# Kernel optimization log

Hardware: AMD Instinct MI355X
Metric: run time of the kernel (lower is better)

## Reference

```python
import jax, jax.numpy as jnp
import numpy as np

N, D, H, E = 8192, 1024, 4096, 8


def setup_inputs() -> dict:
    key = jax.random.key(0)
    ks = jax.random.split(key, 5)
    s_in = 1.0 / np.sqrt(D)
    s_h = 1.0 / np.sqrt(H)
    return {
        "x": jax.random.normal(ks[0], (N, D), dtype=jnp.float32),
        "Wg": jax.random.normal(ks[1], (D, E), dtype=jnp.float32) * s_in,
        "bg": jnp.zeros((E,), dtype=jnp.float32),
        "W1": jax.random.normal(ks[2], (E, D, H), dtype=jnp.float32) * s_in,
        "b1": jnp.zeros((E, H), dtype=jnp.float32),
        "W2": jax.random.normal(ks[3], (E, H, D), dtype=jnp.float32) * s_h,
        "b2": jnp.zeros((E, D), dtype=jnp.float32),
    }


def reference(x, Wg, bg, W1, b1, W2, b2):
    # gate: softmax linear router -> weights [N, E]
    weights = jax.nn.softmax(x @ Wg + bg, axis=-1)
    # all experts, batched GEMMs: h [N, E, H]
    h = jax.nn.relu(jnp.einsum("nd,edh->neh", x, W1) + b1)  # Dropout is identity at inference
    outputs = jnp.einsum("neh,ehd->ned", h, W2) + b2         # [N, E, D]
    # weighted combine over experts
    return jnp.einsum("ne,ned->nd", weights, outputs)
```

## Files before the change

### kernel.cpp

```cpp
#include <hip/hip_runtime.h>
#include <hip/hip_bf16.h>

#define DDIM 1024
#define HDIM 4096
#define NEXP 8
#define NROW 8192

typedef __attribute__((ext_vector_type(8))) short s16x8;
typedef __attribute__((ext_vector_type(4))) float f32x4;

using bf16 = __hip_bfloat16;

__device__ __forceinline__ void gload16(const bf16* g, bf16* lds) {
    __builtin_amdgcn_global_load_lds(
        (const __attribute__((address_space(1))) unsigned int*)g,
        (__attribute__((address_space(3))) unsigned int*)lds,
        16, 0, 0);
}

template <int N>
__device__ __forceinline__ void wait_vmcnt() {
    if constexpr (N == 6)      asm volatile("s_waitcnt vmcnt(6)" ::: "memory");
    else if constexpr (N == 3) asm volatile("s_waitcnt vmcnt(3)" ::: "memory");
    else                       asm volatile("s_waitcnt vmcnt(0)" ::: "memory");
}

__global__ void cvt_x_kernel(const float* __restrict__ x, bf16* __restrict__ xb, int total4) {
    int i = blockIdx.x * 256 + threadIdx.x;
    if (i >= total4) return;
    float4 v = ((const float4*)x)[i];
    union { bf16 b[4]; uint2 u; } p;
    p.b[0] = __float2bfloat16(v.x);
    p.b[1] = __float2bfloat16(v.y);
    p.b[2] = __float2bfloat16(v.z);
    p.b[3] = __float2bfloat16(v.w);
    ((uint2*)xb)[i] = p.u;
}

__global__ void transpose_cvt_kernel(const float* __restrict__ in, bf16* __restrict__ out,
                                     int R, int C) {
    __shared__ float tile[32][33];
    const size_t esz = (size_t)R * C;
    const float* src = in + (size_t)blockIdx.z * esz;
    bf16* dst = out + (size_t)blockIdx.z * esz;
    int c0 = blockIdx.x * 32, r0 = blockIdx.y * 32;
    int tx = threadIdx.x & 31, ty = threadIdx.x >> 5;
#pragma unroll
    for (int i = 0; i < 32; i += 8)
        tile[ty + i][tx] = src[(size_t)(r0 + ty + i) * C + (c0 + tx)];
    __syncthreads();
#pragma unroll
    for (int i = 0; i < 32; i += 8)
        dst[(size_t)(c0 + ty + i) * R + (r0 + tx)] = __float2bfloat16(tile[tx][ty + i]);
}

__global__ void gate_kernel(const float* __restrict__ x, const float* __restrict__ Wg,
                            const float* __restrict__ bg, float* __restrict__ wts) {
    int wave = threadIdx.x >> 6, lane = threadIdx.x & 63;
    int n = blockIdx.x * 4 + wave;
    const float* xr = x + (size_t)n * DDIM;
    float acc[NEXP] = {0.f, 0.f, 0.f, 0.f, 0.f, 0.f, 0.f, 0.f};
    for (int d = lane; d < DDIM; d += 64) {
        float xv = xr[d];
        const float* wr = Wg + (size_t)d * NEXP;
#pragma unroll
        for (int e = 0; e < NEXP; ++e) acc[e] += xv * wr[e];
    }
#pragma unroll
    for (int off = 32; off > 0; off >>= 1) {
#pragma unroll
        for (int e = 0; e < NEXP; ++e) acc[e] += __shfl_xor(acc[e], off, 64);
    }
    if (lane == 0) {
        float mx = -1e30f;
#pragma unroll
        for (int e = 0; e < NEXP; ++e) { acc[e] += bg[e]; mx = fmaxf(mx, acc[e]); }
        float s = 0.f;
#pragma unroll
        for (int e = 0; e < NEXP; ++e) { acc[e] = __expf(acc[e] - mx); s += acc[e]; }
        float inv = 1.0f / s;
#pragma unroll
        for (int e = 0; e < NEXP; ++e) wts[(size_t)n * NEXP + e] = acc[e] * inv;
    }
}

__global__ void out_init_kernel(const float* __restrict__ wts, const float* __restrict__ b2,
                                float* __restrict__ out) {
    size_t idx = (size_t)blockIdx.x * 256 + threadIdx.x;
    int d = (int)(idx & (DDIM - 1));
    size_t n = idx >> 10;
    const float* w = wts + n * NEXP;
    float s = 0.f;
#pragma unroll
    for (int e = 0; e < NEXP; ++e) s += w[e] * b2[(size_t)e * DDIM + d];
    out[idx] = s;
}

template <int BN, int MODE>
__global__ __launch_bounds__(512, 1) void gemm256(
    const bf16* __restrict__ A, const bf16* __restrict__ BT, void* __restrict__ Cout,
    const float* __restrict__ bias, const float* __restrict__ wts,
    int lda, int ldb, int ldc, int NT, int tilesM, int tilesN, int XGN, int expert) {
    constexpr int WN = BN / 64, WM = 8 / WN;
    constexpr int WROWS = 256 / WM;
    constexpr int MH = WROWS / 64;
    constexpr int HALFA = 256 * 32;
    constexpr int HALFB = BN * 32;
    constexpr int ATOT = 2 * HALFA;
    constexpr int BUFE = ATOT + 2 * HALFB;
    constexpr int BR = BN / 128;
    constexpr int VMC = (BN == 256) ? 6 : 3;
    __shared__ __align__(16) bf16 smem[2 * BUFE];

    const int tid = threadIdx.x;
    const int wave = tid >> 6, lane = tid & 63;
    const int wm = wave / WN, wn = wave % WN;
    const int r = lane & 15, kg = lane >> 4;

    const int xcd = blockIdx.x & 7, slot = blockIdx.x >> 3;
    const int XGM = 8 / XGN;
    const int rm = tilesM / XGM, rn = tilesN / XGN;
    const int g = slot >> 5, u = slot & 31;
    const int gpr = rn >> 3;
    const int gm = (g / gpr) * 4 + (u >> 3);
    const int gn = (g % gpr) * 8 + (u & 7);
    const int tm = (xcd / XGN) * rm + gm;
    const int tn = (xcd % XGN) * rn + gn;

    const bf16* gA = A + (size_t)tm * 256 * lda;
    const bf16* gB = BT + (size_t)tn * BN * ldb;

    f32x4 acc[4 * MH][4];
#pragma unroll
    for (int m = 0; m < 4 * MH; ++m)
#pragma unroll
        for (int n = 0; n < 4; ++n) acc[m][n] = (f32x4){0.f, 0.f, 0.f, 0.f};

    auto stageA = [&](int t, int ks) {
        bf16* dst = smem + (t & 1) * BUFE + ks * HALFA;
#pragma unroll
        for (int j = 0; j < 2; ++j) {
            int c = j * 512 + tid;
            int R = c >> 2, kc = (c & 3) ^ ((R >> 1) & 3);
            gload16(gA + (size_t)R * lda + t * 64 + ks * 32 + kc * 8,
                    dst + (j * 512 + wave * 64) * 8);
        }
    };
    auto stageB = [&](int t, int ks) {
        bf16* dst = smem + (t & 1) * BUFE + ATOT + ks * HALFB;
#pragma unroll
        for (int j = 0; j < BR; ++j) {
            int c = j * 512 + tid;
            int R = c >> 2, kc = (c & 3) ^ ((R >> 1) & 3);
            gload16(gB + (size_t)R * ldb + t * 64 + ks * 32 + kc * 8,
                    dst + (j * 512 + wave * 64) * 8);
        }
    };

    s16x8 a0[4], bb[4];
    auto ldA = [&](int buf, int ks, int mh) {
#pragma unroll
        for (int m = 0; m < 4; ++m) {
            int R = wm * WROWS + mh * 64 + m * 16 + r;
            a0[m] = *(const s16x8*)&smem[buf * BUFE + ks * HALFA + R * 32 +
                                         ((kg ^ ((R >> 1) & 3)) * 8)];
        }
    };
    auto ldB = [&](int buf, int ks) {
#pragma unroll
        for (int n = 0; n < 4; ++n) {
            int R = wn * 64 + n * 16 + r;
            bb[n] = *(const s16x8*)&smem[buf * BUFE + ATOT + ks * HALFB + R * 32 +
                                         ((kg ^ ((R >> 1) & 3)) * 8)];
        }
    };

    auto preMFMA = [&]() {
        __builtin_amdgcn_s_barrier();
        asm volatile("s_waitcnt lgkmcnt(0)" ::: "memory");
        __builtin_amdgcn_sched_barrier(0);
        __builtin_amdgcn_s_setprio(1);
    };
    auto postMFMA = [&](bool vm) {
        __builtin_amdgcn_s_setprio(0);
        if (vm) wait_vmcnt<VMC>();
        __builtin_amdgcn_s_barrier();
    };
    auto mfmaLo = [&]() {
#pragma unroll
        for (int m = 0; m < 4; ++m)
#pragma unroll
            for (int n = 0; n < 4; ++n)
                acc[m][n] = __builtin_amdgcn_mfma_f32_16x16x32_bf16(a0[m], bb[n], acc[m][n], 0, 0, 0);
    };
    auto mfmaHi = [&]() {
#pragma unroll
        for (int m = 0; m < 4; ++m)
#pragma unroll
            for (int n = 0; n < 4; ++n)
                acc[4 + m][n] = __builtin_amdgcn_mfma_f32_16x16x32_bf16(a0[m], bb[n], acc[4 + m][n], 0, 0, 0);
    };

    if constexpr (MH == 2) {
        stageB(0, 0); stageA(0, 0); stageB(0, 1); stageA(0, 1);
        stageB(1, 0); stageA(1, 0); stageB(1, 1);
    } else {
        stageA(0, 0); stageB(0, 0); stageA(0, 1); stageB(0, 1);
        stageA(1, 0); stageB(1, 0);
    }
    wait_vmcnt<VMC>();
    __builtin_amdgcn_s_barrier();

    const int NI = NT / 2;
    for (int i = 0; i < NI; ++i) {
        const int t0 = 2 * i, t1 = t0 + 1;
        const bool g2 = (t0 + 2 < NT), g3 = (t1 + 2 < NT);
        if constexpr (MH == 2) {
            ldB(0, 0); ldA(0, 0, 0); stageA(t1, 1);
            preMFMA(); mfmaLo(); postMFMA(false);
            ldA(0, 0, 1); if (g2) stageB(t0 + 2, 0);
            preMFMA(); mfmaHi(); postMFMA(false);
            ldB(0, 1); ldA(0, 1, 0); if (g2) stageA(t0 + 2, 0);
            preMFMA(); mfmaLo(); postMFMA(false);
            ldA(0, 1, 1); if (g2) stageB(t0 + 2, 1);
            preMFMA(); mfmaHi(); postMFMA(true);
            ldB(1, 0); ldA(1, 0, 0); if (g2) stageA(t0 + 2, 1);
            preMFMA(); mfmaLo(); postMFMA(false);
            ldA(1, 0, 1); if (g3) stageB(t1 + 2, 0);
            preMFMA(); mfmaHi(); postMFMA(false);
            ldB(1, 1); ldA(1, 1, 0); if (g3) stageA(t1 + 2, 0);
            preMFMA(); mfmaLo(); postMFMA(false);
            ldA(1, 1, 1); if (g3) stageB(t1 + 2, 1);
            preMFMA(); mfmaHi(); postMFMA(true);
        } else {
            ldB(0, 0); ldA(0, 0, 0); stageA(t1, 1); stageB(t1, 1);
            preMFMA(); mfmaLo(); postMFMA(false);
            ldB(0, 1); ldA(0, 1, 0); if (g2) { stageA(t0 + 2, 0); stageB(t0 + 2, 0); }
            preMFMA(); mfmaLo(); postMFMA(true);
            ldB(1, 0); ldA(1, 0, 0); if (g2) { stageA(t0 + 2, 1); stageB(t0 + 2, 1); }
            preMFMA(); mfmaLo(); postMFMA(false);
            ldB(1, 1); ldA(1, 1, 0); if (g3) { stageA(t1 + 2, 0); stageB(t1 + 2, 0); }
            preMFMA(); mfmaLo(); postMFMA(true);
        }
    }

    if (MODE == 1) {
        bf16* hs = smem;
        const int col0 = tn * BN + wn * 64;
#pragma unroll
        for (int n = 0; n < 4; ++n) {
            float bv = bias[col0 + n * 16 + r];
            int cl = wn * 64 + n * 16 + r;
#pragma unroll
            for (int mf = 0; mf < 4 * MH; ++mf) {
#pragma unroll
                for (int j = 0; j < 4; ++j) {
                    int rl = wm * WROWS + (mf >> 2) * 64 + (mf & 3) * 16 + kg * 4 + j;
                    float v = acc[mf][n][j] + bv;
                    v = v > 0.f ? v : 0.f;
                    hs[rl * 256 + cl] = __float2bfloat16(v);
                }
            }
        }
        __builtin_amdgcn_s_barrier();
        asm volatile("s_waitcnt lgkmcnt(0)" ::: "memory");
        bf16* H = (bf16*)Cout;
        const size_t rbase = (size_t)tm * 256;
        const int cbase = tn * BN;
#pragma unroll
        for (int i2 = 0; i2 < 16; ++i2) {
            int rl = wave * 32 + i2 * 2 + (lane >> 5);
            int c8 = (lane & 31) * 8;
            s16x8 v = *(const s16x8*)&hs[rl * 256 + c8];
            *(s16x8*)&H[(rbase + rl) * (size_t)ldc + cbase + c8] = v;
        }
    } else {
        float* O = (float*)Cout;
        const size_t row0 = (size_t)tm * 256 + wm * WROWS;
        const int col0 = tn * BN + wn * 64;
#pragma unroll
        for (int mf = 0; mf < 4 * MH; ++mf) {
#pragma unroll
            for (int j = 0; j < 4; ++j) {
                size_t rr = row0 + (mf >> 2) * 64 + (mf & 3) * 16 + kg * 4 + j;
                float wv = wts[rr * NEXP + expert];
#pragma unroll
                for (int n = 0; n < 4; ++n) {
                    int cc = col0 + n * 16 + r;
                    O[rr * (size_t)ldc + cc] += wv * acc[mf][n][j];
                }
            }
        }
    }
}

extern "C" void kernel_launch(void* const* d_in, const int* in_sizes, int n_in,
                              void* d_out, int out_size, void* d_ws, size_t ws_size,
                              hipStream_t stream) {
    const float* x  = (const float*)d_in[0];
    const float* Wg = (const float*)d_in[1];
    const float* bg = (const float*)d_in[2];
    const float* W1 = (const float*)d_in[3];
    const float* b1 = (const float*)d_in[4];
    const float* W2 = (const float*)d_in[5];
    const float* b2 = (const float*)d_in[6];
    float* out = (float*)d_out;

    char* ws = (char*)d_ws;
    bf16* xb   = (bf16*)(ws);
    bf16* W1T  = (bf16*)(ws + (16ull << 20));
    bf16* W2T  = (bf16*)(ws + (80ull << 20));
    bf16* Hb   = (bf16*)(ws + (144ull << 20));
    float* wts = (float*)(ws + (208ull << 20));

    cvt_x_kernel<<<(NROW * DDIM / 4 + 255) / 256, 256, 0, stream>>>(x, xb, NROW * DDIM / 4);
    transpose_cvt_kernel<<<dim3(HDIM / 32, DDIM / 32, NEXP), 256, 0, stream>>>(W1, W1T, DDIM, HDIM);
    transpose_cvt_kernel<<<dim3(DDIM / 32, HDIM / 32, NEXP), 256, 0, stream>>>(W2, W2T, HDIM, DDIM);
    gate_kernel<<<NROW / 4, 256, 0, stream>>>(x, Wg, bg, wts);
    out_init_kernel<<<NROW * DDIM / 256, 256, 0, stream>>>(wts, b2, out);

    for (int e = 0; e < NEXP; ++e) {
        gemm256<256, 1><<<512, 512, 0, stream>>>(
            xb, W1T + (size_t)e * HDIM * DDIM, Hb, b1 + (size_t)e * HDIM, nullptr,
            DDIM, DDIM, HDIM, DDIM / 64, 32, 16, 2, e);
        gemm256<128, 2><<<256, 512, 0, stream>>>(
            Hb, W2T + (size_t)e * DDIM * HDIM, out, nullptr, wts,
            HDIM, HDIM, DDIM, HDIM / 64, 32, 8, 1, e);
    }
}
```

Baseline: 1.396 ms.

## Pair experts into one K=8192 down-projection GEMM with gate-weighted hidden and split-K waves

The first GEMM now multiplies the gate weight into the ReLU hidden activations, so two experts' hidden tiles can be concatenated along K and reduced by a single second GEMM per expert pair. This halves the number of read-modify-write passes over the fp32 output. The second GEMM splits K across wave pairs, reduces the partial sums through LDS and uses triple-buffered staging. Weight transpose and conversion is now done per expert inside the loop into small reused buffers, which shrinks the workspace. In exchange, the gate weight is applied before the bf16 rounding of the hidden activations, which slightly changes numerics, and there are more small launches.

```diff
diff --git a/kernel.cpp b/kernel.cpp
--- a/kernel.cpp
+++ b/kernel.cpp
@@ -5,6 +5,7 @@
 #define HDIM 4096
 #define NEXP 8
 #define NROW 8192
+#define KPAIR 8192
 
 typedef __attribute__((ext_vector_type(8))) short s16x8;
 typedef __attribute__((ext_vector_type(4))) float f32x4;
@@ -37,12 +38,9 @@
     ((uint2*)xb)[i] = p.u;
 }
 
-__global__ void transpose_cvt_kernel(const float* __restrict__ in, bf16* __restrict__ out,
-                                     int R, int C) {
+__global__ void transpose_cvt_kernel(const float* __restrict__ src, bf16* __restrict__ dst,
+                                     int R, int C, int ldo) {
     __shared__ float tile[32][33];
-    const size_t esz = (size_t)R * C;
-    const float* src = in + (size_t)blockIdx.z * esz;
-    bf16* dst = out + (size_t)blockIdx.z * esz;
     int c0 = blockIdx.x * 32, r0 = blockIdx.y * 32;
     int tx = threadIdx.x & 31, ty = threadIdx.x >> 5;
 #pragma unroll
@@ -51,7 +49,7 @@
     __syncthreads();
 #pragma unroll
     for (int i = 0; i < 32; i += 8)
-        dst[(size_t)(c0 + ty + i) * R + (r0 + tx)] = __float2bfloat16(tile[tx][ty + i]);
+        dst[(size_t)(c0 + ty + i) * ldo + (r0 + tx)] = __float2bfloat16(tile[tx][ty + i]);
 }
 
 __global__ void gate_kernel(const float* __restrict__ x, const float* __restrict__ Wg,
@@ -96,25 +94,20 @@
     out[idx] = s;
 }
 
-template <int BN, int MODE>
-__global__ __launch_bounds__(512, 1) void gemm256(
-    const bf16* __restrict__ A, const bf16* __restrict__ BT, void* __restrict__ Cout,
+__global__ __launch_bounds__(512, 1) void gemm1(
+    const bf16* __restrict__ A, const bf16* __restrict__ BT, bf16* __restrict__ Cout,
     const float* __restrict__ bias, const float* __restrict__ wts,
     int lda, int ldb, int ldc, int NT, int tilesM, int tilesN, int XGN, int expert) {
-    constexpr int WN = BN / 64, WM = 8 / WN;
-    constexpr int WROWS = 256 / WM;
-    constexpr int MH = WROWS / 64;
+    constexpr int WROWS = 128;
     constexpr int HALFA = 256 * 32;
-    constexpr int HALFB = BN * 32;
+    constexpr int HALFB = 256 * 32;
     constexpr int ATOT = 2 * HALFA;
     constexpr int BUFE = ATOT + 2 * HALFB;
-    constexpr int BR = BN / 128;
-    constexpr int VMC = (BN == 256) ? 6 : 3;
     __shared__ __align__(16) bf16 smem[2 * BUFE];
 
     const int tid = threadIdx.x;
     const int wave = tid >> 6, lane = tid & 63;
-    const int wm = wave / WN, wn = wave % WN;
+    const int wm = wave >> 2, wn = wave & 3;
     const int r = lane & 15, kg = lane >> 4;
 
     const int xcd = blockIdx.x & 7, slot = blockIdx.x >> 3;
@@ -128,11 +121,11 @@
     const int tn = (xcd % XGN) * rn + gn;
 
     const bf16* gA = A + (size_t)tm * 256 * lda;
-    const bf16* gB = BT + (size_t)tn * BN * ldb;
-
-    f32x4 acc[4 * MH][4];
-#pragma unroll
-    for (int m = 0; m < 4 * MH; ++m)
+    const bf16* gB = BT + (size_t)tn * 256 * ldb;
+
+    f32x4 acc[8][4];
+#pragma unroll
+    for (int m = 0; m < 8; ++m)
 #pragma unroll
         for (int n = 0; n < 4; ++n) acc[m][n] = (f32x4){0.f, 0.f, 0.f, 0.f};
 
@@ -149,7 +142,7 @@
     auto stageB = [&](int t, int ks) {
         bf16* dst = smem + (t & 1) * BUFE + ATOT + ks * HALFB;
 #pragma unroll
-        for (int j = 0; j < BR; ++j) {
+        for (int j = 0; j < 2; ++j) {
             int c = j * 512 + tid;
             int R = c >> 2, kc = (c & 3) ^ ((R >> 1) & 3);
             gload16(gB + (size_t)R * ldb + t * 64 + ks * 32 + kc * 8,
@@ -183,7 +176,7 @@
     };
     auto postMFMA = [&](bool vm) {
         __builtin_amdgcn_s_setprio(0);
-        if (vm) wait_vmcnt<VMC>();
+        if (vm) wait_vmcnt<6>();
         __builtin_amdgcn_s_barrier();
     };
     auto mfmaLo = [&]() {
@@ -201,93 +194,202 @@
                 acc[4 + m][n] = __builtin_amdgcn_mfma_f32_16x16x32_bf16(a0[m], bb[n], acc[4 + m][n], 0, 0, 0);
     };
 
-    if constexpr (MH == 2) {
-        stageB(0, 0); stageA(0, 0); stageB(0, 1); stageA(0, 1);
-        stageB(1, 0); stageA(1, 0); stageB(1, 1);
-    } else {
-        stageA(0, 0); stageB(0, 0); stageA(0, 1); stageB(0, 1);
-        stageA(1, 0); stageB(1, 0);
-    }
-    wait_vmcnt<VMC>();
+    stageB(0, 0); stageA(0, 0); stageB(0, 1); stageA(0, 1);
+    stageB(1, 0); stageA(1, 0); stageB(1, 1);
+    wait_vmcnt<6>();
     __builtin_amdgcn_s_barrier();
 
     const int NI = NT / 2;
     for (int i = 0; i < NI; ++i) {
         const int t0 = 2 * i, t1 = t0 + 1;
         const bool g2 = (t0 + 2 < NT), g3 = (t1 + 2 < NT);
-        if constexpr (MH == 2) {
-            ldB(0, 0); ldA(0, 0, 0); stageA(t1, 1);
-            preMFMA(); mfmaLo(); postMFMA(false);
-            ldA(0, 0, 1); if (g2) stageB(t0 + 2, 0);
-            preMFMA(); mfmaHi(); postMFMA(false);
-            ldB(0, 1); ldA(0, 1, 0); if (g2) stageA(t0 + 2, 0);
-            preMFMA(); mfmaLo(); postMFMA(false);
-            ldA(0, 1, 1); if (g2) stageB(t0 + 2, 1);
-            preMFMA(); mfmaHi(); postMFMA(true);
-            ldB(1, 0); ldA(1, 0, 0); if (g2) stageA(t0 + 2, 1);
-            preMFMA(); mfmaLo(); postMFMA(false);
-            ldA(1, 0, 1); if (g3) stageB(t1 + 2, 0);
-            preMFMA(); mfmaHi(); postMFMA(false);
-            ldB(1, 1); ldA(1, 1, 0); if (g3) stageA(t1 + 2, 0);
-            preMFMA(); mfmaLo(); postMFMA(false);
-            ldA(1, 1, 1); if (g3) stageB(t1 + 2, 1);
-            preMFMA(); mfmaHi(); postMFMA(true);
-        } else {
-            ldB(0, 0); ldA(0, 0, 0); stageA(t1, 1); stageB(t1, 1);
-            preMFMA(); mfmaLo(); postMFMA(false);
-            ldB(0, 1); ldA(0, 1, 0); if (g2) { stageA(t0 + 2, 0); stageB(t0 + 2, 0); }
-            preMFMA(); mfmaLo(); postMFMA(true);
-            ldB(1, 0); ldA(1, 0, 0); if (g2) { stageA(t0 + 2, 1); stageB(t0 + 2, 1); }
-            preMFMA(); mfmaLo(); postMFMA(false);
-            ldB(1, 1); ldA(1, 1, 0); if (g3) { stageA(t1 + 2, 0); stageB(t1 + 2, 0); }
-            preMFMA(); mfmaLo(); postMFMA(true);
-        }
-    }
-
-    if (MODE == 1) {
-        bf16* hs = smem;
-        const int col0 = tn * BN + wn * 64;
+        ldB(0, 0); ldA(0, 0, 0); stageA(t1, 1);
+        preMFMA(); mfmaLo(); postMFMA(false);
+        ldA(0, 0, 1); if (g2) stageB(t0 + 2, 0);
+        preMFMA(); mfmaHi(); postMFMA(false);
+        ldB(0, 1); ldA(0, 1, 0); if (g2) stageA(t0 + 2, 0);
+        preMFMA(); mfmaLo(); postMFMA(false);
+        ldA(0, 1, 1); if (g2) stageB(t0 + 2, 1);
+        preMFMA(); mfmaHi(); postMFMA(true);
+        ldB(1, 0); ldA(1, 0, 0); if (g2) stageA(t0 + 2, 1);
+        preMFMA(); mfmaLo(); postMFMA(false);
+        ldA(1, 0, 1); if (g3) stageB(t1 + 2, 0);
+        preMFMA(); mfmaHi(); postMFMA(false);
+        ldB(1, 1); ldA(1, 1, 0); if (g3) stageA(t1 + 2, 0);
+        preMFMA(); mfmaLo(); postMFMA(false);
+        ldA(1, 1, 1); if (g3) stageB(t1 + 2, 1);
+        preMFMA(); mfmaHi(); postMFMA(true);
+    }
+
+    bf16* hs = smem;
+    const int col0 = tn * 256 + wn * 64;
+#pragma unroll
+    for (int n = 0; n < 4; ++n) {
+        float bv = bias[col0 + n * 16 + r];
+        int cl = wn * 64 + n * 16 + r;
+#pragma unroll
+        for (int mf = 0; mf < 8; ++mf) {
+#pragma unroll
+            for (int j = 0; j < 4; ++j) {
+                int rl = wm * WROWS + (mf >> 2) * 64 + (mf & 3) * 16 + kg * 4 + j;
+                float wv = wts[((size_t)tm * 256 + rl) * NEXP + expert];
+                float v = acc[mf][n][j] + bv;
+                v = v > 0.f ? v : 0.f;
+                hs[rl * 256 + cl] = __float2bfloat16(wv * v);
+            }
+        }
+    }
+    __builtin_amdgcn_s_barrier();
+    asm volatile("s_waitcnt lgkmcnt(0)" ::: "memory");
+    const size_t rbase = (size_t)tm * 256;
+    const int cbase = tn * 256;
+#pragma unroll
+    for (int i2 = 0; i2 < 16; ++i2) {
+        int rl = wave * 32 + i2 * 2 + (lane >> 5);
+        int c8 = (lane & 31) * 8;
+        s16x8 v = *(const s16x8*)&hs[rl * 256 + c8];
+        *(s16x8*)&Cout[(rbase + rl) * (size_t)ldc + cbase + c8] = v;
+    }
+}
+
+__global__ __launch_bounds__(512, 1) void gemm2pair(
+    const bf16* __restrict__ A, const bf16* __restrict__ BT, float* __restrict__ O,
+    int lda, int ldb, int ldc, int NT, int tilesM, int tilesN, int XGN) {
+    constexpr int HALFA = 256 * 32;
+    constexpr int HALFB = 128 * 32;
+    constexpr int ATOT = 2 * HALFA;
+    constexpr int BUFE = ATOT + 2 * HALFB;
+    __shared__ __align__(16) bf16 smem[3 * BUFE];
+
+    const int tid = threadIdx.x;
+    const int wave = tid >> 6, lane = tid & 63;
+    const int ksw = wave & 1, wn = (wave >> 1) & 1, wm = wave >> 2;
+    const int r = lane & 15, kg = lane >> 4;
+
+    const int xcd = blockIdx.x & 7, slot = blockIdx.x >> 3;
+    const int XGM = 8 / XGN;
+    const int rm = tilesM / XGM, rn = tilesN / XGN;
+    const int g = slot >> 5, u = slot & 31;
+    const int gpr = rn >> 3;
+    const int gm = (g / gpr) * 4 + (u >> 3);
+    const int gn = (g % gpr) * 8 + (u & 7);
+    const int tm = (xcd / XGN) * rm + gm;
+    const int tn = (xcd % XGN) * rn + gn;
+
+    const bf16* gA = A + (size_t)tm * 256 * lda;
+    const bf16* gB = BT + (size_t)tn * 128 * ldb;
+
+    f32x4 acc[8][4];
+#pragma unroll
+    for (int m = 0; m < 8; ++m)
+#pragma unroll
+        for (int n = 0; n < 4; ++n) acc[m][n] = (f32x4){0.f, 0.f, 0.f, 0.f};
+
+    auto stageA = [&](int t, int ks) {
+        bf16* dst = smem + (t % 3) * BUFE + ks * HALFA;
+#pragma unroll
+        for (int j = 0; j < 2; ++j) {
+            int c = j * 512 + tid;
+            int R = c >> 2, kc = (c & 3) ^ ((R >> 1) & 3);
+            gload16(gA + (size_t)R * lda + t * 64 + ks * 32 + kc * 8,
+                    dst + (j * 512 + wave * 64) * 8);
+        }
+    };
+    auto stageB = [&](int t, int ks) {
+        bf16* dst = smem + (t % 3) * BUFE + ATOT + ks * HALFB;
+        int R = tid >> 2, kc = (tid & 3) ^ ((R >> 1) & 3);
+        gload16(gB + (size_t)R * ldb + t * 64 + ks * 32 + kc * 8, dst + (wave * 64) * 8);
+    };
+
+    s16x8 afr[4], bfr[4];
+    auto ldA = [&](int rb, int mh) {
+#pragma unroll
+        for (int m = 0; m < 4; ++m) {
+            int R = wm * 128 + mh * 64 + m * 16 + r;
+            afr[m] = *(const s16x8*)&smem[rb * BUFE + ksw * HALFA + R * 32 +
+                                          ((kg ^ ((R >> 1) & 3)) * 8)];
+        }
+    };
+    auto ldB = [&](int rb) {
 #pragma unroll
         for (int n = 0; n < 4; ++n) {
-            float bv = bias[col0 + n * 16 + r];
-            int cl = wn * 64 + n * 16 + r;
-#pragma unroll
-            for (int mf = 0; mf < 4 * MH; ++mf) {
-#pragma unroll
-                for (int j = 0; j < 4; ++j) {
-                    int rl = wm * WROWS + (mf >> 2) * 64 + (mf & 3) * 16 + kg * 4 + j;
-                    float v = acc[mf][n][j] + bv;
-                    v = v > 0.f ? v : 0.f;
-                    hs[rl * 256 + cl] = __float2bfloat16(v);
-                }
-            }
-        }
+            int R = wn * 64 + n * 16 + r;
+            bfr[n] = *(const s16x8*)&smem[rb * BUFE + ATOT + ksw * HALFB + R * 32 +
+                                          ((kg ^ ((R >> 1) & 3)) * 8)];
+        }
+    };
+    auto preMFMA = [&]() {
         __builtin_amdgcn_s_barrier();
         asm volatile("s_waitcnt lgkmcnt(0)" ::: "memory");
-        bf16* H = (bf16*)Cout;
-        const size_t rbase = (size_t)tm * 256;
-        const int cbase = tn * BN;
-#pragma unroll
-        for (int i2 = 0; i2 < 16; ++i2) {
-            int rl = wave * 32 + i2 * 2 + (lane >> 5);
-            int c8 = (lane & 31) * 8;
-            s16x8 v = *(const s16x8*)&hs[rl * 256 + c8];
-            *(s16x8*)&H[(rbase + rl) * (size_t)ldc + cbase + c8] = v;
-        }
-    } else {
-        float* O = (float*)Cout;
-        const size_t row0 = (size_t)tm * 256 + wm * WROWS;
-        const int col0 = tn * BN + wn * 64;
-#pragma unroll
-        for (int mf = 0; mf < 4 * MH; ++mf) {
+        __builtin_amdgcn_sched_barrier(0);
+        __builtin_amdgcn_s_setprio(1);
+    };
+
+    stageA(0, 0); stageB(0, 0); stageA(0, 1); stageB(0, 1);
+    stageA(1, 0); stageB(1, 0); stageA(1, 1); stageB(1, 1);
+    wait_vmcnt<6>();
+    __builtin_amdgcn_s_barrier();
+
+    for (int t = 0; t < NT; ++t) {
+        const int rb = t % 3;
+        const bool gg = (t + 2 < NT);
+        ldB(rb); ldA(rb, 0);
+        if (gg) { stageA(t + 2, 0); stageB(t + 2, 0); }
+        preMFMA();
+#pragma unroll
+        for (int m = 0; m < 4; ++m)
+#pragma unroll
+            for (int n = 0; n < 4; ++n)
+                acc[m][n] = __builtin_amdgcn_mfma_f32_16x16x32_bf16(afr[m], bfr[n], acc[m][n], 0, 0, 0);
+        __builtin_amdgcn_s_setprio(0);
+        __builtin_amdgcn_s_barrier();
+        ldA(rb, 1);
+        if (gg) { stageA(t + 2, 1); stageB(t + 2, 1); }
+        preMFMA();
+#pragma unroll
+        for (int m = 0; m < 4; ++m)
+#pragma unroll
+            for (int n = 0; n < 4; ++n)
+                acc[4 + m][n] = __builtin_amdgcn_mfma_f32_16x16x32_bf16(afr[m], bfr[n], acc[4 + m][n], 0, 0, 0);
+        __builtin_amdgcn_s_setprio(0);
+        if (t + 1 < NT) {
+            if (gg) wait_vmcnt<6>();
+            else    wait_vmcnt<0>();
+            __builtin_amdgcn_s_barrier();
+        }
+    }
+
+    __syncthreads();
+    float* red = (float*)smem;
+    const int zone = (wm * 2 + wn) * 8192;
+    if (ksw == 1) {
+#pragma unroll
+        for (int mf = 0; mf < 8; ++mf) {
+#pragma unroll
+            for (int n = 0; n < 4; ++n) {
+                int rl = (mf >> 2) * 64 + (mf & 3) * 16 + kg * 4;
+                int cl = n * 16 + r;
+#pragma unroll
+                for (int j = 0; j < 4; ++j)
+                    red[zone + (rl + j) * 64 + cl] = acc[mf][n][j];
+            }
+        }
+    }
+    __syncthreads();
+    if (ksw == 0) {
+        const size_t row0 = (size_t)tm * 256 + wm * 128;
+        const int col0 = tn * 128 + wn * 64;
+#pragma unroll
+        for (int mf = 0; mf < 8; ++mf) {
 #pragma unroll
             for (int j = 0; j < 4; ++j) {
-                size_t rr = row0 + (mf >> 2) * 64 + (mf & 3) * 16 + kg * 4 + j;
-                float wv = wts[rr * NEXP + expert];
+                int rl = (mf >> 2) * 64 + (mf & 3) * 16 + kg * 4 + j;
+                size_t rr = row0 + rl;
 #pragma unroll
                 for (int n = 0; n < 4; ++n) {
-                    int cc = col0 + n * 16 + r;
-                    O[rr * (size_t)ldc + cc] += wv * acc[mf][n][j];
+                    int cl = n * 16 + r;
+                    float v = acc[mf][n][j] + red[zone + rl * 64 + cl];
+                    O[rr * (size_t)ldc + col0 + cl] += v;
                 }
             }
         }
@@ -308,23 +410,27 @@
 
     char* ws = (char*)d_ws;
     bf16* xb   = (bf16*)(ws);
-    bf16* W1T  = (bf16*)(ws + (16ull << 20));
-    bf16* W2T  = (bf16*)(ws + (80ull << 20));
-    bf16* Hb   = (bf16*)(ws + (144ull << 20));
-    float* wts = (float*)(ws + (208ull << 20));
-
-    cvt_x_kernel<<<(NROW * DDIM / 4 + 255) / 256, 256, 0, stream>>>(x, xb, NROW * DDIM / 4);
-    transpose_cvt_kernel<<<dim3(HDIM / 32, DDIM / 32, NEXP), 256, 0, stream>>>(W1, W1T, DDIM, HDIM);
-    transpose_cvt_kernel<<<dim3(DDIM / 32, HDIM / 32, NEXP), 256, 0, stream>>>(W2, W2T, HDIM, DDIM);
+    bf16* W1Te = (bf16*)(ws + (16ull << 20));
+    bf16* W2P  = (bf16*)(ws + (24ull << 20));
+    bf16* Hs   = (bf16*)(ws + (40ull << 20));
+    float* wts = (float*)(ws + (168ull << 20));
+
+    cvt_x_kernel<<<NROW * DDIM / 4 / 256, 256, 0, stream>>>(x, xb, NROW * DDIM / 4);
     gate_kernel<<<NROW / 4, 256, 0, stream>>>(x, Wg, bg, wts);
     out_init_kernel<<<NROW * DDIM / 256, 256, 0, stream>>>(wts, b2, out);
 
-    for (int e = 0; e < NEXP; ++e) {
-        gemm256<256, 1><<<512, 512, 0, stream>>>(
-            xb, W1T + (size_t)e * HDIM * DDIM, Hb, b1 + (size_t)e * HDIM, nullptr,
-            DDIM, DDIM, HDIM, DDIM / 64, 32, 16, 2, e);
-        gemm256<128, 2><<<256, 512, 0, stream>>>(
-            Hb, W2T + (size_t)e * DDIM * HDIM, out, nullptr, wts,
-            HDIM, HDIM, DDIM, HDIM / 64, 32, 8, 1, e);
-    }
-}
+    for (int p = 0; p < 4; ++p) {
+        for (int h = 0; h < 2; ++h) {
+            int e = 2 * p + h;
+            transpose_cvt_kernel<<<dim3(HDIM / 32, DDIM / 32), 256, 0, stream>>>(
+                W1 + (size_t)e * DDIM * HDIM, W1Te, DDIM, HDIM, DDIM);
+            gemm1<<<512, 512, 0, stream>>>(
+                xb, W1Te, Hs + (size_t)h * HDIM, b1 + (size_t)e * HDIM, wts,
+                DDIM, DDIM, KPAIR, DDIM / 64, 32, 16, 2, e);
+            transpose_cvt_kernel<<<dim3(DDIM / 32, HDIM / 32), 256, 0, stream>>>(
+                W2 + (size_t)e * HDIM * DDIM, W2P + (size_t)h * HDIM, HDIM, DDIM, KPAIR);
+        }
+        gemm2pair<<<256, 512, 0, stream>>>(
+            Hs, W2P, out, KPAIR, KPAIR, DDIM, KPAIR / 64, 32, 8, 1);
+    }
+}
```

Result: faster. 1.337 ms (-4.2%).

## Pair experts into K=8192 down-proj GEMM with split-K and fused gate scaling

Applied to the files above, without the earlier changes.

Folds the gate weight into the ReLU output of the up-projection, which lets two experts' hidden activations be concatenated along K. One down-projection GEMM with 256x256 tiles and a two-way split-K (scratch buffer plus a final combine kernel) then replaces the per-expert 128-wide GEMMs. Weight transposes now run per expert or per pair, interleaved with the GEMMs into small workspace buffers, and use a wider vectorized transpose. This cuts read-modify-write traffic on the fp32 output and the number of launches, at the cost of an extra scratch pass and the hidden activations being quantized to bf16 after the gate weight is applied.

```diff
diff --git a/kernel.cpp b/kernel.cpp
--- a/kernel.cpp
+++ b/kernel.cpp
@@ -5,6 +5,7 @@
 #define HDIM 4096
 #define NEXP 8
 #define NROW 8192
+#define KPAIR 8192
 
 typedef __attribute__((ext_vector_type(8))) short s16x8;
 typedef __attribute__((ext_vector_type(4))) float f32x4;
@@ -37,21 +38,33 @@
     ((uint2*)xb)[i] = p.u;
 }
 
-__global__ void transpose_cvt_kernel(const float* __restrict__ in, bf16* __restrict__ out,
-                                     int R, int C) {
-    __shared__ float tile[32][33];
-    const size_t esz = (size_t)R * C;
-    const float* src = in + (size_t)blockIdx.z * esz;
-    bf16* dst = out + (size_t)blockIdx.z * esz;
-    int c0 = blockIdx.x * 32, r0 = blockIdx.y * 32;
-    int tx = threadIdx.x & 31, ty = threadIdx.x >> 5;
-#pragma unroll
-    for (int i = 0; i < 32; i += 8)
-        tile[ty + i][tx] = src[(size_t)(r0 + ty + i) * C + (c0 + tx)];
+__global__ void transpose_cvt_kernel(const float* __restrict__ src, bf16* __restrict__ dst,
+                                     int R, int C, int ldo, size_t szs, int dzo) {
+    __shared__ float t[128][65];
+    const float* s = src + (size_t)blockIdx.z * szs;
+    bf16* d = dst + (size_t)blockIdx.z * dzo;
+    const int r0 = blockIdx.y * 64, c0 = blockIdx.x * 128;
+    const int tid = threadIdx.x;
+    const int lrow = tid >> 5, lc4 = tid & 31;
+#pragma unroll
+    for (int i = 0; i < 8; ++i) {
+        int rr = i * 8 + lrow;
+        float4 v = *(const float4*)&s[(size_t)(r0 + rr) * C + c0 + lc4 * 4];
+        t[lc4 * 4 + 0][rr] = v.x;
+        t[lc4 * 4 + 1][rr] = v.y;
+        t[lc4 * 4 + 2][rr] = v.z;
+        t[lc4 * 4 + 3][rr] = v.w;
+    }
     __syncthreads();
-#pragma unroll
-    for (int i = 0; i < 32; i += 8)
-        dst[(size_t)(c0 + ty + i) * R + (r0 + tx)] = __float2bfloat16(tile[tx][ty + i]);
+    const int oc = tid >> 3, oj = tid & 7;
+#pragma unroll
+    for (int i = 0; i < 4; ++i) {
+        int c = oc + i * 32;
+        union { bf16 b[8]; s16x8 v; } p;
+#pragma unroll
+        for (int q = 0; q < 8; ++q) p.b[q] = __float2bfloat16(t[c][oj * 8 + q]);
+        *(s16x8*)&d[(size_t)(c0 + c) * ldo + r0 + oj * 8] = p.v;
+    }
 }
 
 __global__ void gate_kernel(const float* __restrict__ x, const float* __restrict__ Wg,
@@ -96,25 +109,30 @@
     out[idx] = s;
 }
 
-template <int BN, int MODE>
+__global__ void combine_kernel(float* __restrict__ out, const float* __restrict__ osc) {
+    size_t i = (size_t)blockIdx.x * 256 + threadIdx.x;
+    float4 a = ((const float4*)out)[i];
+    float4 b = ((const float4*)osc)[i];
+    a.x += b.x; a.y += b.y; a.z += b.z; a.w += b.w;
+    ((float4*)out)[i] = a;
+}
+
+template <int MODE>
 __global__ __launch_bounds__(512, 1) void gemm256(
     const bf16* __restrict__ A, const bf16* __restrict__ BT, void* __restrict__ Cout,
-    const float* __restrict__ bias, const float* __restrict__ wts,
-    int lda, int ldb, int ldc, int NT, int tilesM, int tilesN, int XGN, int expert) {
-    constexpr int WN = BN / 64, WM = 8 / WN;
-    constexpr int WROWS = 256 / WM;
-    constexpr int MH = WROWS / 64;
+    float* __restrict__ Oalt, const float* __restrict__ bias, const float* __restrict__ wts,
+    int lda, int ldb, int ldc, int NT, int tilesM, int tilesN, int XGN,
+    int expert, int first) {
+    constexpr int WROWS = 128;
     constexpr int HALFA = 256 * 32;
-    constexpr int HALFB = BN * 32;
+    constexpr int HALFB = 256 * 32;
     constexpr int ATOT = 2 * HALFA;
     constexpr int BUFE = ATOT + 2 * HALFB;
-    constexpr int BR = BN / 128;
-    constexpr int VMC = (BN == 256) ? 6 : 3;
     __shared__ __align__(16) bf16 smem[2 * BUFE];
 
     const int tid = threadIdx.x;
     const int wave = tid >> 6, lane = tid & 63;
-    const int wm = wave / WN, wn = wave % WN;
+    const int wm = wave >> 2, wn = wave & 3;
     const int r = lane & 15, kg = lane >> 4;
 
     const int xcd = blockIdx.x & 7, slot = blockIdx.x >> 3;
@@ -125,14 +143,18 @@
     const int gm = (g / gpr) * 4 + (u >> 3);
     const int gn = (g % gpr) * 8 + (u & 7);
     const int tm = (xcd / XGN) * rm + gm;
-    const int tn = (xcd % XGN) * rn + gn;
-
-    const bf16* gA = A + (size_t)tm * 256 * lda;
-    const bf16* gB = BT + (size_t)tn * BN * ldb;
-
-    f32x4 acc[4 * MH][4];
-#pragma unroll
-    for (int m = 0; m < 4 * MH; ++m)
+    const int tn_v = (xcd % XGN) * rn + gn;
+
+    int kh = 0, tn = tn_v;
+    if constexpr (MODE == 2) { kh = tn_v >> 2; tn = tn_v & 3; }
+    const int kofs = kh * NT * 64;
+
+    const bf16* gA = A + (size_t)tm * 256 * lda + kofs;
+    const bf16* gB = BT + (size_t)tn * 256 * ldb + kofs;
+
+    f32x4 acc[8][4];
+#pragma unroll
+    for (int m = 0; m < 8; ++m)
 #pragma unroll
         for (int n = 0; n < 4; ++n) acc[m][n] = (f32x4){0.f, 0.f, 0.f, 0.f};
 
@@ -149,7 +171,7 @@
     auto stageB = [&](int t, int ks) {
         bf16* dst = smem + (t & 1) * BUFE + ATOT + ks * HALFB;
 #pragma unroll
-        for (int j = 0; j < BR; ++j) {
+        for (int j = 0; j < 2; ++j) {
             int c = j * 512 + tid;
             int R = c >> 2, kc = (c & 3) ^ ((R >> 1) & 3);
             gload16(gB + (size_t)R * ldb + t * 64 + ks * 32 + kc * 8,
@@ -183,7 +205,7 @@
     };
     auto postMFMA = [&](bool vm) {
         __builtin_amdgcn_s_setprio(0);
-        if (vm) wait_vmcnt<VMC>();
+        if (vm) wait_vmcnt<6>();
         __builtin_amdgcn_s_barrier();
     };
     auto mfmaLo = [&]() {
@@ -201,64 +223,49 @@
                 acc[4 + m][n] = __builtin_amdgcn_mfma_f32_16x16x32_bf16(a0[m], bb[n], acc[4 + m][n], 0, 0, 0);
     };
 
-    if constexpr (MH == 2) {
-        stageB(0, 0); stageA(0, 0); stageB(0, 1); stageA(0, 1);
-        stageB(1, 0); stageA(1, 0); stageB(1, 1);
-    } else {
-        stageA(0, 0); stageB(0, 0); stageA(0, 1); stageB(0, 1);
-        stageA(1, 0); stageB(1, 0);
-    }
-    wait_vmcnt<VMC>();
+    stageB(0, 0); stageA(0, 0); stageB(0, 1); stageA(0, 1);
+    stageB(1, 0); stageA(1, 0); stageB(1, 1);
+    wait_vmcnt<6>();
     __builtin_amdgcn_s_barrier();
 
     const int NI = NT / 2;
     for (int i = 0; i < NI; ++i) {
         const int t0 = 2 * i, t1 = t0 + 1;
         const bool g2 = (t0 + 2 < NT), g3 = (t1 + 2 < NT);
-        if constexpr (MH == 2) {
-            ldB(0, 0); ldA(0, 0, 0); stageA(t1, 1);
-            preMFMA(); mfmaLo(); postMFMA(false);
-            ldA(0, 0, 1); if (g2) stageB(t0 + 2, 0);
-            preMFMA(); mfmaHi(); postMFMA(false);
-            ldB(0, 1); ldA(0, 1, 0); if (g2) stageA(t0 + 2, 0);
-            preMFMA(); mfmaLo(); postMFMA(false);
-            ldA(0, 1, 1); if (g2) stageB(t0 + 2, 1);
-            preMFMA(); mfmaHi(); postMFMA(true);
-            ldB(1, 0); ldA(1, 0, 0); if (g2) stageA(t0 + 2, 1);
-            preMFMA(); mfmaLo(); postMFMA(false);
-            ldA(1, 0, 1); if (g3) stageB(t1 + 2, 0);
-            preMFMA(); mfmaHi(); postMFMA(false);
-            ldB(1, 1); ldA(1, 1, 0); if (g3) stageA(t1 + 2, 0);
-            preMFMA(); mfmaLo(); postMFMA(false);
-            ldA(1, 1, 1); if (g3) stageB(t1 + 2, 1);
-            preMFMA(); mfmaHi(); postMFMA(true);
-        } else {
-            ldB(0, 0); ldA(0, 0, 0); stageA(t1, 1); stageB(t1, 1);
-            preMFMA(); mfmaLo(); postMFMA(false);
-            ldB(0, 1); ldA(0, 1, 0); if (g2) { stageA(t0 + 2, 0); stageB(t0 + 2, 0); }
-            preMFMA(); mfmaLo(); postMFMA(true);
-            ldB(1, 0); ldA(1, 0, 0); if (g2) { stageA(t0 + 2, 1); stageB(t0 + 2, 1); }
-            preMFMA(); mfmaLo(); postMFMA(false);
-            ldB(1, 1); ldA(1, 1, 0); if (g3) { stageA(t1 + 2, 0); stageB(t1 + 2, 0); }
-            preMFMA(); mfmaLo(); postMFMA(true);
-        }
-    }
-
-    if (MODE == 1) {
+        ldB(0, 0); ldA(0, 0, 0); stageA(t1, 1);
+        preMFMA(); mfmaLo(); postMFMA(false);
+        ldA(0, 0, 1); if (g2) stageB(t0 + 2, 0);
+        preMFMA(); mfmaHi(); postMFMA(false);
+        ldB(0, 1); ldA(0, 1, 0); if (g2) stageA(t0 + 2, 0);
+        preMFMA(); mfmaLo(); postMFMA(false);
+        ldA(0, 1, 1); if (g2) stageB(t0 + 2, 1);
+        preMFMA(); mfmaHi(); postMFMA(true);
+        ldB(1, 0); ldA(1, 0, 0); if (g2) stageA(t0 + 2, 1);
+        preMFMA(); mfmaLo(); postMFMA(false);
+        ldA(1, 0, 1); if (g3) stageB(t1 + 2, 0);
+        preMFMA(); mfmaHi(); postMFMA(false);
+        ldB(1, 1); ldA(1, 1, 0); if (g3) stageA(t1 + 2, 0);
+        preMFMA(); mfmaLo(); postMFMA(false);
+        ldA(1, 1, 1); if (g3) stageB(t1 + 2, 1);
+        preMFMA(); mfmaHi(); postMFMA(true);
+    }
+
+    if constexpr (MODE == 1) {
         bf16* hs = smem;
-        const int col0 = tn * BN + wn * 64;
+        const int col0 = tn * 256 + wn * 64;
 #pragma unroll
         for (int n = 0; n < 4; ++n) {
             float bv = bias[col0 + n * 16 + r];
             int cl = wn * 64 + n * 16 + r;
 #pragma unroll
-            for (int mf = 0; mf < 4 * MH; ++mf) {
+            for (int mf = 0; mf < 8; ++mf) {
 #pragma unroll
                 for (int j = 0; j < 4; ++j) {
                     int rl = wm * WROWS + (mf >> 2) * 64 + (mf & 3) * 16 + kg * 4 + j;
+                    float wv = wts[((size_t)tm * 256 + rl) * NEXP + expert];
                     float v = acc[mf][n][j] + bv;
                     v = v > 0.f ? v : 0.f;
-                    hs[rl * 256 + cl] = __float2bfloat16(v);
+                    hs[rl * 256 + cl] = __float2bfloat16(wv * v);
                 }
             }
         }
@@ -266,7 +273,7 @@
         asm volatile("s_waitcnt lgkmcnt(0)" ::: "memory");
         bf16* H = (bf16*)Cout;
         const size_t rbase = (size_t)tm * 256;
-        const int cbase = tn * BN;
+        const int cbase = tn * 256;
 #pragma unroll
         for (int i2 = 0; i2 < 16; ++i2) {
             int rl = wave * 32 + i2 * 2 + (lane >> 5);
@@ -275,19 +282,20 @@
             *(s16x8*)&H[(rbase + rl) * (size_t)ldc + cbase + c8] = v;
         }
     } else {
-        float* O = (float*)Cout;
+        float* O = (kh == 0) ? (float*)Cout : Oalt;
+        const bool rmw = (kh == 0) || (first == 0);
         const size_t row0 = (size_t)tm * 256 + wm * WROWS;
-        const int col0 = tn * BN + wn * 64;
-#pragma unroll
-        for (int mf = 0; mf < 4 * MH; ++mf) {
+        const int col0 = tn * 256 + wn * 64;
+#pragma unroll
+        for (int mf = 0; mf < 8; ++mf) {
 #pragma unroll
             for (int j = 0; j < 4; ++j) {
                 size_t rr = row0 + (mf >> 2) * 64 + (mf & 3) * 16 + kg * 4 + j;
-                float wv = wts[rr * NEXP + expert];
 #pragma unroll
                 for (int n = 0; n < 4; ++n) {
-                    int cc = col0 + n * 16 + r;
-                    O[rr * (size_t)ldc + cc] += wv * acc[mf][n][j];
+                    size_t o = rr * (size_t)ldc + col0 + n * 16 + r;
+                    if (rmw) O[o] += acc[mf][n][j];
+                    else     O[o] = acc[mf][n][j];
                 }
             }
         }
@@ -308,23 +316,31 @@
 
     char* ws = (char*)d_ws;
     bf16* xb   = (bf16*)(ws);
-    bf16* W1T  = (bf16*)(ws + (16ull << 20));
-    bf16* W2T  = (bf16*)(ws + (80ull << 20));
-    bf16* Hb   = (bf16*)(ws + (144ull << 20));
-    float* wts = (float*)(ws + (208ull << 20));
-
-    cvt_x_kernel<<<(NROW * DDIM / 4 + 255) / 256, 256, 0, stream>>>(x, xb, NROW * DDIM / 4);
-    transpose_cvt_kernel<<<dim3(HDIM / 32, DDIM / 32, NEXP), 256, 0, stream>>>(W1, W1T, DDIM, HDIM);
-    transpose_cvt_kernel<<<dim3(DDIM / 32, HDIM / 32, NEXP), 256, 0, stream>>>(W2, W2T, HDIM, DDIM);
+    bf16* W1Te = (bf16*)(ws + (16ull << 20));
+    bf16* W2P  = (bf16*)(ws + (24ull << 20));
+    bf16* Hs   = (bf16*)(ws + (40ull << 20));
+    float* Osc = (float*)(ws + (168ull << 20));
+    float* wts = (float*)(ws + (200ull << 20));
+
+    cvt_x_kernel<<<NROW * DDIM / 4 / 256, 256, 0, stream>>>(x, xb, NROW * DDIM / 4);
     gate_kernel<<<NROW / 4, 256, 0, stream>>>(x, Wg, bg, wts);
     out_init_kernel<<<NROW * DDIM / 256, 256, 0, stream>>>(wts, b2, out);
 
-    for (int e = 0; e < NEXP; ++e) {
-        gemm256<256, 1><<<512, 512, 0, stream>>>(
-            xb, W1T + (size_t)e * HDIM * DDIM, Hb, b1 + (size_t)e * HDIM, nullptr,
-            DDIM, DDIM, HDIM, DDIM / 64, 32, 16, 2, e);
-        gemm256<128, 2><<<256, 512, 0, stream>>>(
-            Hb, W2T + (size_t)e * DDIM * HDIM, out, nullptr, wts,
-            HDIM, HDIM, DDIM, HDIM / 64, 32, 8, 1, e);
-    }
-}
+    for (int p = 0; p < 4; ++p) {
+        for (int h = 0; h < 2; ++h) {
+            int e = 2 * p + h;
+            transpose_cvt_kernel<<<dim3(HDIM / 128, DDIM / 64, 1), 256, 0, stream>>>(
+                W1 + (size_t)e * DDIM * HDIM, W1Te, DDIM, HDIM, DDIM, 0, 0);
+            gemm256<1><<<512, 512, 0, stream>>>(
+                xb, W1Te, Hs + (size_t)h * HDIM, nullptr, b1 + (size_t)e * HDIM, wts,
+                DDIM, DDIM, KPAIR, DDIM / 64, 32, 16, 2, e, 0);
+        }
+        transpose_cvt_kernel<<<dim3(DDIM / 128, HDIM / 64, 2), 256, 0, stream>>>(
+            W2 + (size_t)2 * p * HDIM * DDIM, W2P, HDIM, DDIM, KPAIR,
+            (size_t)HDIM * DDIM, HDIM);
+        gemm256<2><<<256, 512, 0, stream>>>(
+            Hs, W2P, out, Osc, nullptr, nullptr,
+            KPAIR, KPAIR, DDIM, 64, 32, 8, 1, 0, (p == 0) ? 1 : 0);
+    }
+    combine_kernel<<<NROW * DDIM / 4 / 256, 256, 0, stream>>>(out, Osc);
+}
```

Result: slower. 1.429 ms (+2.4%).
